# Kernel tuning notes

Hardware: AMD Instinct MI355X
Metric: run time of the kernel (lower is better)

The kernel has to match this reference:

```python
import jax, jax.numpy as jnp
import numpy as np

B, T, H, U, F, K, M = 64, 2048, 1024, 128, 32, 31, 512
PAD = 2 * (K - 1) // 2  # dilation=2, 'same' padding = 30


def setup_inputs() -> dict:
    key = jax.random.key(0)
    ks = jax.random.split(key, 10)
    s = lambda d: 1.0 / np.sqrt(d)
    return {
        "query": jax.random.normal(ks[0], (B, 1, H), dtype=jnp.float32),
        "state": jax.random.uniform(ks[1], (B, T), dtype=jnp.float32),
        "prev_cum": jnp.zeros((B, T), dtype=jnp.float32),
        "memory": jax.random.normal(ks[2], (B, T, M), dtype=jnp.float32),
        "Wq": jax.random.normal(ks[3], (H, U), dtype=jnp.float32) * s(H),
        "bq": jnp.zeros((U,), dtype=jnp.float32),
        "Wm": jax.random.normal(ks[4], (M, U), dtype=jnp.float32) * s(M),
        "bm": jnp.zeros((U,), dtype=jnp.float32),
        "Wl": jax.random.normal(ks[5], (F, U), dtype=jnp.float32) * s(F),
        "bl": jnp.zeros((U,), dtype=jnp.float32),
        "We": jax.random.normal(ks[6], (U, U), dtype=jnp.float32) * s(U),
        "be": jnp.zeros((U,), dtype=jnp.float32),
        "va": jax.random.normal(ks[7], (U,), dtype=jnp.float32),
        "conv_w": jax.random.normal(ks[8], (F, 1, K), dtype=jnp.float32) * s(K),
        "conv_b": jnp.zeros((F,), dtype=jnp.float32),
    }


def reference(query, state, prev_cum, memory, Wq, bq, Wm, bm, Wl, bl, We, be, va, conv_w, conv_b):
    # query projection, keep first time step: [B,1,U]
    pq = (query @ Wq + bq)[:, 0:1, :]
    # processed memory (done in initialize() in torch): [B,T,U]
    pm = memory @ Wm + bm
    # location features: dilated conv over previous alignment, 'same' length
    x = state[:, None, :]  # [B,1,T]
    f = jax.lax.conv_general_dilated(
        x, conv_w, window_strides=(1,), padding=[(PAD, PAD)],
        rhs_dilation=(2,), dimension_numbers=("NCH", "OIH", "NCH"),
    ) + conv_b[None, :, None]                     # [B,F,T]
    pl = jnp.transpose(f, (0, 2, 1)) @ Wl + bl    # [B,T,U]
    # additive energy with extra linear + v_a reduction: [B,T]
    energy = jnp.sum(va * jnp.tanh((pq + pl + pm) @ We + be), axis=2)
    # smoothing (sigmoid) normalization instead of softmax
    sg = jax.nn.sigmoid(energy)
    alignment = sg / jnp.sum(sg, axis=-1, keepdims=True)  # [B,T]
    cum = prev_cum + alignment  # cumulate_weights=True
    # context over PROCESSED memory, matching self.memoery usage: [B,1,U]
    context = cum[:, None, :] @ pm
    return context
```

## Files before the change

### kernel.cpp

```cpp
#include <hip/hip_runtime.h>

#define Bv 64
#define Tv 2048
#define Hv 1024
#define Uv 128
#define Mv 512

typedef __bf16 bf16x8 __attribute__((ext_vector_type(8)));
typedef float f32x4 __attribute__((ext_vector_type(4)));

union U4BF { uint4 u; bf16x8 b; };

#define MFMA(a, b, c) __builtin_amdgcn_mfma_f32_16x16x32_bf16((a), (b), (c), 0, 0, 0)

__device__ __forceinline__ unsigned short f2bf(float f) {
  __bf16 h = (__bf16)f;
  return __builtin_bit_cast(unsigned short, h);
}
__device__ __forceinline__ unsigned int pack2(unsigned short lo, unsigned short hi) {
  return (unsigned int)lo | ((unsigned int)hi << 16);
}

__global__ __launch_bounds__(128) void k1_kernel(const float* __restrict__ query,
                                                 const float* __restrict__ Wq,
                                                 const float* __restrict__ bq,
                                                 const float* __restrict__ Wl,
                                                 const float* __restrict__ bl,
                                                 const float* __restrict__ conv_w,
                                                 const float* __restrict__ conv_b,
                                                 float* __restrict__ pq,
                                                 float* __restrict__ W2,
                                                 float* __restrict__ bias2) {
  const int bx = blockIdx.x;
  const int u = threadIdx.x;
  if (bx < 512) {
    const int b = bx >> 3, c = bx & 7;
    float acc = (c == 0) ? bq[u] : 0.0f;
    const float* q  = query + b * Hv + c * 128;
    const float* wq = Wq + (size_t)c * 128 * Uv;
    #pragma unroll 8
    for (int h = 0; h < 128; ++h) acc = fmaf(q[h], wq[h * Uv + u], acc);
    unsafeAtomicAdd(&pq[b * Uv + u], acc);
  } else {
    float wl[32];
    #pragma unroll
    for (int f = 0; f < 32; ++f) wl[f] = Wl[f * Uv + u];
    for (int k = 0; k < 31; ++k) {
      float acc = 0.0f;
      #pragma unroll
      for (int f = 0; f < 32; ++f) acc = fmaf(conv_w[f * 31 + k], wl[f], acc);
      W2[k * Uv + u] = acc;
    }
    float acc = bl[u];
    #pragma unroll
    for (int f = 0; f < 32; ++f) acc = fmaf(conv_b[f], wl[f], acc);
    bias2[u] = acc;
  }
}

__global__ __launch_bounds__(256) void k2_kernel(const float* __restrict__ pq,
                                                 const float* __restrict__ bias2,
                                                 const float* __restrict__ bm,
                                                 const float* __restrict__ be,
                                                 const float* __restrict__ We,
                                                 const float* __restrict__ W2,
                                                 float* __restrict__ qe,
                                                 float* __restrict__ w3tmp) {
  const int gtid = blockIdx.x * 256 + threadIdx.x;
  const int r = gtid >> 7, n = gtid & 127;
  if (r < 64) {
    float acc = be[n];
    for (int u = 0; u < Uv; ++u)
      acc = fmaf(pq[r * Uv + u] + bias2[u] + bm[u], We[u * Uv + n], acc);
    qe[r * Uv + n] = acc;
  } else {
    const int w = r - 64;
    float acc = 0.0f;
    if (w < 31) {
      for (int u = 0; u < Uv; ++u) acc = fmaf(W2[w * Uv + u], We[u * Uv + n], acc);
    }
    w3tmp[w * Uv + n] = acc;
  }
}

__global__ __launch_bounds__(256) void k3_kernel(const float* __restrict__ Wm,
                                                 const float* __restrict__ We,
                                                 const float* __restrict__ w3tmp,
                                                 unsigned short* __restrict__ WmF,
                                                 unsigned short* __restrict__ WeF,
                                                 unsigned short* __restrict__ W3F) {
  const int gtid = blockIdx.x * 256 + threadIdx.x;
  const int fid = gtid >> 6, lane = gtid & 63;
  const int quad = lane >> 4, l4 = lane & 15;
  float v[8];
  unsigned short* dst;
  if (fid < 128) {
    const int kc = fid >> 3, uj = fid & 7;
    #pragma unroll
    for (int j = 0; j < 8; ++j) v[j] = Wm[(size_t)(kc * 32 + quad * 8 + j) * Uv + uj * 16 + l4];
    dst = WmF + (size_t)fid * 512 + lane * 8;
  } else if (fid < 160) {
    const int f2 = fid - 128;
    const int kc = f2 >> 3, nj = f2 & 7;
    #pragma unroll
    for (int j = 0; j < 8; ++j) v[j] = We[(size_t)(kc * 32 + quad * 8 + j) * Uv + nj * 16 + l4];
    dst = WeF + (size_t)f2 * 512 + lane * 8;
  } else {
    const int nj = fid - 160;
    #pragma unroll
    for (int j = 0; j < 8; ++j) v[j] = w3tmp[(quad * 8 + j) * Uv + nj * 16 + l4];
    dst = W3F + (size_t)nj * 512 + lane * 8;
  }
  uint4 o;
  o.x = pack2(f2bf(v[0]), f2bf(v[1]));
  o.y = pack2(f2bf(v[2]), f2bf(v[3]));
  o.z = pack2(f2bf(v[4]), f2bf(v[5]));
  o.w = pack2(f2bf(v[6]), f2bf(v[7]));
  *(uint4*)dst = o;
}

__global__ __launch_bounds__(256) void main_kernel(
    const float* __restrict__ memory, const unsigned short* __restrict__ WmF,
    const unsigned short* __restrict__ WeF, const unsigned short* __restrict__ W3F,
    const float* __restrict__ qe, const float* __restrict__ state,
    const float* __restrict__ prev_cum, const float* __restrict__ bm,
    const float* __restrict__ va,
    float* __restrict__ P0, float* __restrict__ P1, float* __restrict__ Ssg) {
  const int tid = threadIdx.x;
  const int lane = tid & 63, wid = tid >> 6;
  const int l4 = lane & 15, quad = lane >> 4;
  const int wt = wid >> 1, wu = wid & 1;
  const int b = blockIdx.y, t0 = blockIdx.x * 64;

  __shared__ float sState[124];
  __shared__ float sPc[64];
  __shared__ float sBm[128];
  __shared__ float sVa[128];
  __shared__ float sSg[64];
  __shared__ float blkP0[128], blkP1[128];
  __shared__ float blkSsg;
  __shared__ __align__(16) unsigned short sS[64 * 144];

  for (int i = tid; i < 124; i += 256) {
    int t = t0 - 30 + i;
    sState[i] = (t >= 0 && t < Tv) ? state[b * Tv + t] : 0.0f;
  }
  if (tid < 64) sPc[tid] = prev_cum[b * Tv + t0 + tid];
  for (int i = tid; i < 128; i += 256) {
    sBm[i] = bm[i]; sVa[i] = va[i]; blkP0[i] = 0.0f; blkP1[i] = 0.0f;
  }
  if (tid == 0) blkSsg = 0.0f;

  f32x4 acc[2][4];
  #pragma unroll
  for (int ti = 0; ti < 2; ++ti)
    #pragma unroll
    for (int uj = 0; uj < 4; ++uj) acc[ti][uj] = (f32x4){0.f, 0.f, 0.f, 0.f};

  const float* aBase = memory + ((size_t)b * Tv + t0 + wt * 32 + l4) * Mv + quad * 8;
  const unsigned short* bBase = WmF + (size_t)(wu * 4) * 512 + lane * 8;

  for (int kc = 0; kc < 16; ++kc) {
    float4 a0 = *(const float4*)(aBase + kc * 32);
    float4 a1 = *(const float4*)(aBase + kc * 32 + 4);
    float4 a2 = *(const float4*)(aBase + (size_t)16 * Mv + kc * 32);
    float4 a3 = *(const float4*)(aBase + (size_t)16 * Mv + kc * 32 + 4);
    U4BF bf[4];
    #pragma unroll
    for (int uj = 0; uj < 4; ++uj)
      bf[uj].u = *(const uint4*)(bBase + (size_t)(kc * 8 + uj) * 512);
    bf16x8 af0, af1;
    af0[0] = (__bf16)a0.x; af0[1] = (__bf16)a0.y; af0[2] = (__bf16)a0.z; af0[3] = (__bf16)a0.w;
    af0[4] = (__bf16)a1.x; af0[5] = (__bf16)a1.y; af0[6] = (__bf16)a1.z; af0[7] = (__bf16)a1.w;
    af1[0] = (__bf16)a2.x; af1[1] = (__bf16)a2.y; af1[2] = (__bf16)a2.z; af1[3] = (__bf16)a2.w;
    af1[4] = (__bf16)a3.x; af1[5] = (__bf16)a3.y; af1[6] = (__bf16)a3.z; af1[7] = (__bf16)a3.w;
    #pragma unroll
    for (int uj = 0; uj < 4; ++uj) {
      acc[0][uj] = MFMA(af0, bf[uj].b, acc[0][uj]);
      acc[1][uj] = MFMA(af1, bf[uj].b, acc[1][uj]);
    }
  }

  #pragma unroll
  for (int ti = 0; ti < 2; ++ti) {
    const int rowb = wt * 32 + ti * 16 + quad * 4;
    #pragma unroll
    for (int uj = 0; uj < 4; ++uj) {
      const int col = wu * 64 + uj * 16 + l4;
      #pragma unroll
      for (int r = 0; r < 4; ++r) sS[(rowb + r) * 144 + col] = f2bf(acc[ti][uj][r]);
    }
  }
  __syncthreads();

  const int w = wid;
  f32x4 e[8];
  #pragma unroll
  for (int nj = 0; nj < 8; ++nj) {
    float qv = qe[b * Uv + nj * 16 + l4];
    e[nj] = (f32x4){qv, qv, qv, qv};
  }
  bf16x8 a2f;
  #pragma unroll
  for (int j = 0; j < 8; ++j) {
    int k = quad * 8 + j;
    float v = (k < 31) ? sState[(w * 16 + l4) + 2 * k] : 0.0f;
    a2f[j] = (__bf16)v;
  }
  #pragma unroll
  for (int nj = 0; nj < 8; ++nj) {
    U4BF bb; bb.u = *(const uint4*)(W3F + (size_t)nj * 512 + lane * 8);
    e[nj] = MFMA(a2f, bb.b, e[nj]);
  }
  #pragma unroll
  for (int ks = 0; ks < 4; ++ks) {
    U4BF au;
    au.u = *(const uint4*)&sS[(w * 16 + l4) * 144 + ks * 32 + quad * 8];
    #pragma unroll
    for (int nj = 0; nj < 8; ++nj) {
      U4BF bb; bb.u = *(const uint4*)(WeF + (size_t)(ks * 8 + nj) * 512 + lane * 8);
      e[nj] = MFMA(au.b, bb.b, e[nj]);
    }
  }
  float p[4] = {0.f, 0.f, 0.f, 0.f};
  #pragma unroll
  for (int nj = 0; nj < 8; ++nj) {
    float vav = sVa[nj * 16 + l4];
    #pragma unroll
    for (int r = 0; r < 4; ++r) p[r] = fmaf(vav, tanhf(e[nj][r]), p[r]);
  }
  #pragma unroll
  for (int off = 1; off <= 8; off <<= 1) {
    #pragma unroll
    for (int r = 0; r < 4; ++r) p[r] += __shfl_xor(p[r], off, 64);
  }
  float sgv4[4], sgsum = 0.f;
  #pragma unroll
  for (int r = 0; r < 4; ++r) {
    sgv4[r] = 1.0f / (1.0f + expf(-p[r]));
    sgsum += sgv4[r];
  }
  if (l4 == 0) {
    #pragma unroll
    for (int r = 0; r < 4; ++r) sSg[w * 16 + quad * 4 + r] = sgv4[r];
    atomicAdd(&blkSsg, sgsum);
  }
  __syncthreads();

  float sgl[8], pcl[8];
  #pragma unroll
  for (int ti = 0; ti < 2; ++ti)
    #pragma unroll
    for (int r = 0; r < 4; ++r) {
      int row = wt * 32 + ti * 16 + quad * 4 + r;
      sgl[ti * 4 + r] = sSg[row];
      pcl[ti * 4 + r] = sPc[row];
    }
  #pragma unroll
  for (int uj = 0; uj < 4; ++uj) {
    const int col = wu * 64 + uj * 16 + l4;
    const float bmv = sBm[col];
    float c0 = 0.f, c1 = 0.f;
    #pragma unroll
    for (int ti = 0; ti < 2; ++ti)
      #pragma unroll
      for (int r = 0; r < 4; ++r) {
        float pmv = acc[ti][uj][r] + bmv;
        c0 = fmaf(pcl[ti * 4 + r], pmv, c0);
        c1 = fmaf(sgl[ti * 4 + r], pmv, c1);
      }
    c0 += __shfl_xor(c0, 16, 64); c0 += __shfl_xor(c0, 32, 64);
    c1 += __shfl_xor(c1, 16, 64); c1 += __shfl_xor(c1, 32, 64);
    if (quad == 0) {
      atomicAdd(&blkP0[col], c0);
      atomicAdd(&blkP1[col], c1);
    }
  }
  __syncthreads();
  if (tid < 128) {
    unsafeAtomicAdd(&P0[b * Uv + tid], blkP0[tid]);
    unsafeAtomicAdd(&P1[b * Uv + tid], blkP1[tid]);
  }
  if (tid == 0) unsafeAtomicAdd(&Ssg[b], blkSsg);
}

__global__ __launch_bounds__(128) void finish_kernel(const float* __restrict__ P0,
                                                     const float* __restrict__ P1,
                                                     const float* __restrict__ Ssg,
                                                     float* __restrict__ out) {
  const int b = blockIdx.x, u = threadIdx.x;
  out[b * Uv + u] = P0[b * Uv + u] + P1[b * Uv + u] / Ssg[b];
}

extern "C" void kernel_launch(void* const* d_in, const int* in_sizes, int n_in,
                              void* d_out, int out_size, void* d_ws, size_t ws_size,
                              hipStream_t stream) {
  (void)in_sizes; (void)n_in; (void)out_size; (void)ws_size;
  const float* query    = (const float*)d_in[0];
  const float* state    = (const float*)d_in[1];
  const float* prev_cum = (const float*)d_in[2];
  const float* memory   = (const float*)d_in[3];
  const float* Wq       = (const float*)d_in[4];
  const float* bq       = (const float*)d_in[5];
  const float* Wm       = (const float*)d_in[6];
  const float* bm       = (const float*)d_in[7];
  const float* Wl       = (const float*)d_in[8];
  const float* bl       = (const float*)d_in[9];
  const float* We       = (const float*)d_in[10];
  const float* be       = (const float*)d_in[11];
  const float* va       = (const float*)d_in[12];
  const float* conv_w   = (const float*)d_in[13];
  const float* conv_b   = (const float*)d_in[14];

  float* ws = (float*)d_ws;
  float* P0    = ws;
  float* P1    = ws + 8192;
  float* Ssg   = ws + 16384;
  float* pq    = ws + 16448;
  float* W2    = ws + 24640;
  float* bias2 = ws + 28608;
  float* qe    = ws + 28736;
  float* w3tmp = ws + 36928;
  unsigned short* WmF = (unsigned short*)(ws + 41024);
  unsigned short* WeF = (unsigned short*)(ws + 73792);
  unsigned short* W3F = (unsigned short*)(ws + 81984);

  hipMemsetAsync(d_ws, 0, 24640 * sizeof(float), stream);

  k1_kernel<<<513, 128, 0, stream>>>(query, Wq, bq, Wl, bl, conv_w, conv_b, pq, W2, bias2);
  k2_kernel<<<48, 256, 0, stream>>>(pq, bias2, bm, be, We, W2, qe, w3tmp);
  k3_kernel<<<42, 256, 0, stream>>>(Wm, We, w3tmp, WmF, WeF, W3F);
  main_kernel<<<dim3(Tv / 64, Bv), 256, 0, stream>>>(
      memory, WmF, WeF, W3F, qe, state, prev_cum, bm, va, P0, P1, Ssg);
  finish_kernel<<<Bv, 128, 0, stream>>>(P0, P1, Ssg, (float*)d_out);
}
```

Before: 465.4 us.

## Merge prep kernels, fuse finish via last-block counter, double-buffer GEMM loads

Replaces the memset and three setup kernels with a single prep kernel that also zeroes the accumulation workspace. The separate finish kernel is removed: each batch row counts finished blocks with an atomic counter, and the last block writes the output. The main GEMM loop now double-buffers memory and weight loads in registers. It also prefetches the W3 and qe operands, shrinks the LDS row padding, and uses fast exp-based tanh and sigmoid. The aim is fewer launches and better latency hiding, at the cost of higher register pressure and slightly lower transcendental accuracy.

```diff
diff --git a/kernel.cpp b/kernel.cpp
--- a/kernel.cpp
+++ b/kernel.cpp
@@ -8,9 +8,7 @@
 
 typedef __bf16 bf16x8 __attribute__((ext_vector_type(8)));
 typedef float f32x4 __attribute__((ext_vector_type(4)));
-
 union U4BF { uint4 u; bf16x8 b; };
-
 #define MFMA(a, b, c) __builtin_amdgcn_mfma_f32_16x16x32_bf16((a), (b), (c), 0, 0, 0)
 
 __device__ __forceinline__ unsigned short f2bf(float f) {
@@ -20,112 +18,119 @@
 __device__ __forceinline__ unsigned int pack2(unsigned short lo, unsigned short hi) {
   return (unsigned int)lo | ((unsigned int)hi << 16);
 }
-
-__global__ __launch_bounds__(128) void k1_kernel(const float* __restrict__ query,
-                                                 const float* __restrict__ Wq,
-                                                 const float* __restrict__ bq,
-                                                 const float* __restrict__ Wl,
-                                                 const float* __restrict__ bl,
-                                                 const float* __restrict__ conv_w,
-                                                 const float* __restrict__ conv_b,
-                                                 float* __restrict__ pq,
-                                                 float* __restrict__ W2,
-                                                 float* __restrict__ bias2) {
-  const int bx = blockIdx.x;
-  const int u = threadIdx.x;
-  if (bx < 512) {
-    const int b = bx >> 3, c = bx & 7;
-    float acc = (c == 0) ? bq[u] : 0.0f;
-    const float* q  = query + b * Hv + c * 128;
-    const float* wq = Wq + (size_t)c * 128 * Uv;
-    #pragma unroll 8
-    for (int h = 0; h < 128; ++h) acc = fmaf(q[h], wq[h * Uv + u], acc);
-    unsafeAtomicAdd(&pq[b * Uv + u], acc);
+__device__ __forceinline__ float fast_tanh(float x) {
+  x = fminf(fmaxf(x, -15.0f), 15.0f);
+  float e = __expf(2.0f * x);
+  return (e - 1.0f) / (e + 1.0f);
+}
+
+__global__ __launch_bounds__(256) void prep_kernel(
+    const float* __restrict__ query, const float* __restrict__ Wq,
+    const float* __restrict__ bq, const float* __restrict__ Wl,
+    const float* __restrict__ bl, const float* __restrict__ conv_w,
+    const float* __restrict__ conv_b, const float* __restrict__ bm,
+    const float* __restrict__ be, const float* __restrict__ We,
+    const float* __restrict__ Wm,
+    float* __restrict__ qe, unsigned short* __restrict__ W3F,
+    unsigned short* __restrict__ WmF, unsigned short* __restrict__ WeF,
+    float* __restrict__ zeroRegion) {
+  const int bx = blockIdx.x, tid = threadIdx.x;
+  if (bx < 64) {
+    const int b = bx;
+    __shared__ float part[256];
+    __shared__ float svec[128];
+    const int u = tid & 127, half = tid >> 7;
+    float acc = 0.0f;
+    const float* q  = query + b * Hv + half * 512;
+    const float* wq = Wq + (size_t)(half * 512) * Uv + u;
+    for (int h = 0; h < 512; ++h) acc = fmaf(q[h], wq[(size_t)h * Uv], acc);
+    part[tid] = acc;
+    __syncthreads();
+    if (tid < 128) {
+      float pq = part[tid] + part[tid + 128] + bq[tid];
+      float b2 = bl[tid];
+      #pragma unroll
+      for (int f = 0; f < 32; ++f) b2 = fmaf(conv_b[f], Wl[f * Uv + tid], b2);
+      svec[tid] = pq + b2 + bm[tid];
+    }
+    __syncthreads();
+    const int n = tid & 127;
+    float acc2 = 0.0f;
+    const float* we = We + (size_t)(half * 64) * Uv + n;
+    for (int uu = 0; uu < 64; ++uu) acc2 = fmaf(svec[half * 64 + uu], we[(size_t)uu * Uv], acc2);
+    part[tid] = acc2;
+    __syncthreads();
+    if (tid < 128) qe[b * Uv + tid] = part[tid] + part[tid + 128] + be[tid];
+  } else if (bx == 64) {
+    __shared__ float sW2[31 * 128];
+    __shared__ float sW3[32 * 128];
+    for (int idx = tid; idx < 31 * 128; idx += 256) {
+      int k = idx >> 7, uu = idx & 127;
+      float a = 0.0f;
+      #pragma unroll
+      for (int f = 0; f < 32; ++f) a = fmaf(conv_w[f * 31 + k], Wl[f * Uv + uu], a);
+      sW2[idx] = a;
+    }
+    __syncthreads();
+    for (int idx = tid; idx < 32 * 128; idx += 256) {
+      int k = idx >> 7, n = idx & 127;
+      float a = 0.0f;
+      if (k < 31) {
+        for (int uu = 0; uu < 128; ++uu) a = fmaf(sW2[k * 128 + uu], We[(size_t)uu * Uv + n], a);
+      }
+      sW3[idx] = a;
+    }
+    __syncthreads();
+    for (int s = tid; s < 512; s += 256) {
+      int nj = s >> 6, lane = s & 63, quad = lane >> 4, l4 = lane & 15;
+      float v[8];
+      #pragma unroll
+      for (int j = 0; j < 8; ++j) v[j] = sW3[(quad * 8 + j) * 128 + nj * 16 + l4];
+      uint4 o;
+      o.x = pack2(f2bf(v[0]), f2bf(v[1])); o.y = pack2(f2bf(v[2]), f2bf(v[3]));
+      o.z = pack2(f2bf(v[4]), f2bf(v[5])); o.w = pack2(f2bf(v[6]), f2bf(v[7]));
+      *(uint4*)(W3F + (size_t)nj * 512 + lane * 8) = o;
+    }
+  } else if (bx < 97) {
+    const int fid = (bx - 65) * 4 + (tid >> 6);
+    const int lane = tid & 63, quad = lane >> 4, l4 = lane & 15;
+    const int kc = fid >> 3, uj = fid & 7;
+    float v[8];
+    #pragma unroll
+    for (int j = 0; j < 8; ++j) v[j] = Wm[(size_t)(kc * 32 + quad * 8 + j) * Uv + uj * 16 + l4];
+    uint4 o;
+    o.x = pack2(f2bf(v[0]), f2bf(v[1])); o.y = pack2(f2bf(v[2]), f2bf(v[3]));
+    o.z = pack2(f2bf(v[4]), f2bf(v[5])); o.w = pack2(f2bf(v[6]), f2bf(v[7]));
+    *(uint4*)(WmF + (size_t)fid * 512 + lane * 8) = o;
+  } else if (bx < 105) {
+    const int f2 = (bx - 97) * 4 + (tid >> 6);
+    const int lane = tid & 63, quad = lane >> 4, l4 = lane & 15;
+    const int ks = f2 >> 3, nj = f2 & 7;
+    float v[8];
+    #pragma unroll
+    for (int j = 0; j < 8; ++j) v[j] = We[(size_t)(ks * 32 + quad * 8 + j) * Uv + nj * 16 + l4];
+    uint4 o;
+    o.x = pack2(f2bf(v[0]), f2bf(v[1])); o.y = pack2(f2bf(v[2]), f2bf(v[3]));
+    o.z = pack2(f2bf(v[4]), f2bf(v[5])); o.w = pack2(f2bf(v[6]), f2bf(v[7]));
+    *(uint4*)(WeF + (size_t)f2 * 512 + lane * 8) = o;
   } else {
-    float wl[32];
-    #pragma unroll
-    for (int f = 0; f < 32; ++f) wl[f] = Wl[f * Uv + u];
-    for (int k = 0; k < 31; ++k) {
-      float acc = 0.0f;
-      #pragma unroll
-      for (int f = 0; f < 32; ++f) acc = fmaf(conv_w[f * 31 + k], wl[f], acc);
-      W2[k * Uv + u] = acc;
-    }
-    float acc = bl[u];
-    #pragma unroll
-    for (int f = 0; f < 32; ++f) acc = fmaf(conv_b[f], wl[f], acc);
-    bias2[u] = acc;
-  }
-}
-
-__global__ __launch_bounds__(256) void k2_kernel(const float* __restrict__ pq,
-                                                 const float* __restrict__ bias2,
-                                                 const float* __restrict__ bm,
-                                                 const float* __restrict__ be,
-                                                 const float* __restrict__ We,
-                                                 const float* __restrict__ W2,
-                                                 float* __restrict__ qe,
-                                                 float* __restrict__ w3tmp) {
-  const int gtid = blockIdx.x * 256 + threadIdx.x;
-  const int r = gtid >> 7, n = gtid & 127;
-  if (r < 64) {
-    float acc = be[n];
-    for (int u = 0; u < Uv; ++u)
-      acc = fmaf(pq[r * Uv + u] + bias2[u] + bm[u], We[u * Uv + n], acc);
-    qe[r * Uv + n] = acc;
-  } else {
-    const int w = r - 64;
-    float acc = 0.0f;
-    if (w < 31) {
-      for (int u = 0; u < Uv; ++u) acc = fmaf(W2[w * Uv + u], We[u * Uv + n], acc);
-    }
-    w3tmp[w * Uv + n] = acc;
-  }
-}
-
-__global__ __launch_bounds__(256) void k3_kernel(const float* __restrict__ Wm,
-                                                 const float* __restrict__ We,
-                                                 const float* __restrict__ w3tmp,
-                                                 unsigned short* __restrict__ WmF,
-                                                 unsigned short* __restrict__ WeF,
-                                                 unsigned short* __restrict__ W3F) {
-  const int gtid = blockIdx.x * 256 + threadIdx.x;
-  const int fid = gtid >> 6, lane = gtid & 63;
-  const int quad = lane >> 4, l4 = lane & 15;
-  float v[8];
-  unsigned short* dst;
-  if (fid < 128) {
-    const int kc = fid >> 3, uj = fid & 7;
-    #pragma unroll
-    for (int j = 0; j < 8; ++j) v[j] = Wm[(size_t)(kc * 32 + quad * 8 + j) * Uv + uj * 16 + l4];
-    dst = WmF + (size_t)fid * 512 + lane * 8;
-  } else if (fid < 160) {
-    const int f2 = fid - 128;
-    const int kc = f2 >> 3, nj = f2 & 7;
-    #pragma unroll
-    for (int j = 0; j < 8; ++j) v[j] = We[(size_t)(kc * 32 + quad * 8 + j) * Uv + nj * 16 + l4];
-    dst = WeF + (size_t)f2 * 512 + lane * 8;
-  } else {
-    const int nj = fid - 160;
-    #pragma unroll
-    for (int j = 0; j < 8; ++j) v[j] = w3tmp[(quad * 8 + j) * Uv + nj * 16 + l4];
-    dst = W3F + (size_t)nj * 512 + lane * 8;
-  }
-  uint4 o;
-  o.x = pack2(f2bf(v[0]), f2bf(v[1]));
-  o.y = pack2(f2bf(v[2]), f2bf(v[3]));
-  o.z = pack2(f2bf(v[4]), f2bf(v[5]));
-  o.w = pack2(f2bf(v[6]), f2bf(v[7]));
-  *(uint4*)dst = o;
-}
-
-__global__ __launch_bounds__(256) void main_kernel(
+    const int base = (bx - 105) * 2048 + tid * 8;
+    if (base < 16512) {
+      float4 z = {0.f, 0.f, 0.f, 0.f};
+      *(float4*)(zeroRegion + base) = z;
+      *(float4*)(zeroRegion + base + 4) = z;
+    }
+  }
+}
+
+__global__ __launch_bounds__(256, 4) void main_kernel(
     const float* __restrict__ memory, const unsigned short* __restrict__ WmF,
     const unsigned short* __restrict__ WeF, const unsigned short* __restrict__ W3F,
     const float* __restrict__ qe, const float* __restrict__ state,
     const float* __restrict__ prev_cum, const float* __restrict__ bm,
     const float* __restrict__ va,
-    float* __restrict__ P0, float* __restrict__ P1, float* __restrict__ Ssg) {
+    float* __restrict__ P0, float* __restrict__ P1, float* __restrict__ Ssg,
+    int* __restrict__ cnt, float* __restrict__ out) {
   const int tid = threadIdx.x;
   const int lane = tid & 63, wid = tid >> 6;
   const int l4 = lane & 15, quad = lane >> 4;
@@ -139,16 +144,15 @@
   __shared__ float sSg[64];
   __shared__ float blkP0[128], blkP1[128];
   __shared__ float blkSsg;
-  __shared__ __align__(16) unsigned short sS[64 * 144];
+  __shared__ int sDone;
+  __shared__ __align__(16) unsigned short sS[64 * 136];
 
   for (int i = tid; i < 124; i += 256) {
     int t = t0 - 30 + i;
     sState[i] = (t >= 0 && t < Tv) ? state[b * Tv + t] : 0.0f;
   }
   if (tid < 64) sPc[tid] = prev_cum[b * Tv + t0 + tid];
-  for (int i = tid; i < 128; i += 256) {
-    sBm[i] = bm[i]; sVa[i] = va[i]; blkP0[i] = 0.0f; blkP1[i] = 0.0f;
-  }
+  if (tid < 128) { sBm[tid] = bm[tid]; sVa[tid] = va[tid]; blkP0[tid] = 0.0f; blkP1[tid] = 0.0f; }
   if (tid == 0) blkSsg = 0.0f;
 
   f32x4 acc[2][4];
@@ -157,28 +161,54 @@
     #pragma unroll
     for (int uj = 0; uj < 4; ++uj) acc[ti][uj] = (f32x4){0.f, 0.f, 0.f, 0.f};
 
-  const float* aBase = memory + ((size_t)b * Tv + t0 + wt * 32 + l4) * Mv + quad * 8;
-  const unsigned short* bBase = WmF + (size_t)(wu * 4) * 512 + lane * 8;
-
+  const float* aPtr = memory + ((size_t)b * Tv + t0 + wt * 32 + l4) * Mv + quad * 8;
+  const unsigned short* bPtr = WmF + (size_t)(wu * 4) * 512 + lane * 8;
+
+  float4 Abuf[2][4];
+  uint4  Bbuf[2][4];
+  Abuf[0][0] = *(const float4*)(aPtr);
+  Abuf[0][1] = *(const float4*)(aPtr + 4);
+  Abuf[0][2] = *(const float4*)(aPtr + (size_t)16 * Mv);
+  Abuf[0][3] = *(const float4*)(aPtr + (size_t)16 * Mv + 4);
+  #pragma unroll
+  for (int j = 0; j < 4; ++j) Bbuf[0][j] = *(const uint4*)(bPtr + (size_t)j * 512);
+
+  #pragma unroll
   for (int kc = 0; kc < 16; ++kc) {
-    float4 a0 = *(const float4*)(aBase + kc * 32);
-    float4 a1 = *(const float4*)(aBase + kc * 32 + 4);
-    float4 a2 = *(const float4*)(aBase + (size_t)16 * Mv + kc * 32);
-    float4 a3 = *(const float4*)(aBase + (size_t)16 * Mv + kc * 32 + 4);
-    U4BF bf[4];
-    #pragma unroll
-    for (int uj = 0; uj < 4; ++uj)
-      bf[uj].u = *(const uint4*)(bBase + (size_t)(kc * 8 + uj) * 512);
+    const int cur = kc & 1, nxt = cur ^ 1;
+    if (kc < 15) {
+      const float* ap = aPtr + (kc + 1) * 32;
+      Abuf[nxt][0] = *(const float4*)(ap);
+      Abuf[nxt][1] = *(const float4*)(ap + 4);
+      Abuf[nxt][2] = *(const float4*)(ap + (size_t)16 * Mv);
+      Abuf[nxt][3] = *(const float4*)(ap + (size_t)16 * Mv + 4);
+      #pragma unroll
+      for (int j = 0; j < 4; ++j)
+        Bbuf[nxt][j] = *(const uint4*)(bPtr + (size_t)((kc + 1) * 8 + j) * 512);
+    }
     bf16x8 af0, af1;
-    af0[0] = (__bf16)a0.x; af0[1] = (__bf16)a0.y; af0[2] = (__bf16)a0.z; af0[3] = (__bf16)a0.w;
-    af0[4] = (__bf16)a1.x; af0[5] = (__bf16)a1.y; af0[6] = (__bf16)a1.z; af0[7] = (__bf16)a1.w;
-    af1[0] = (__bf16)a2.x; af1[1] = (__bf16)a2.y; af1[2] = (__bf16)a2.z; af1[3] = (__bf16)a2.w;
-    af1[4] = (__bf16)a3.x; af1[5] = (__bf16)a3.y; af1[6] = (__bf16)a3.z; af1[7] = (__bf16)a3.w;
+    af0[0] = (__bf16)Abuf[cur][0].x; af0[1] = (__bf16)Abuf[cur][0].y;
+    af0[2] = (__bf16)Abuf[cur][0].z; af0[3] = (__bf16)Abuf[cur][0].w;
+    af0[4] = (__bf16)Abuf[cur][1].x; af0[5] = (__bf16)Abuf[cur][1].y;
+    af0[6] = (__bf16)Abuf[cur][1].z; af0[7] = (__bf16)Abuf[cur][1].w;
+    af1[0] = (__bf16)Abuf[cur][2].x; af1[1] = (__bf16)Abuf[cur][2].y;
+    af1[2] = (__bf16)Abuf[cur][2].z; af1[3] = (__bf16)Abuf[cur][2].w;
+    af1[4] = (__bf16)Abuf[cur][3].x; af1[5] = (__bf16)Abuf[cur][3].y;
+    af1[6] = (__bf16)Abuf[cur][3].z; af1[7] = (__bf16)Abuf[cur][3].w;
     #pragma unroll
     for (int uj = 0; uj < 4; ++uj) {
-      acc[0][uj] = MFMA(af0, bf[uj].b, acc[0][uj]);
-      acc[1][uj] = MFMA(af1, bf[uj].b, acc[1][uj]);
-    }
+      U4BF bb; bb.u = Bbuf[cur][uj];
+      acc[0][uj] = MFMA(af0, bb.b, acc[0][uj]);
+      acc[1][uj] = MFMA(af1, bb.b, acc[1][uj]);
+    }
+  }
+
+  float qv[8];
+  U4BF w3[8];
+  #pragma unroll
+  for (int nj = 0; nj < 8; ++nj) {
+    qv[nj] = qe[b * Uv + nj * 16 + l4];
+    w3[nj].u = *(const uint4*)(W3F + (size_t)nj * 512 + lane * 8);
   }
 
   #pragma unroll
@@ -188,34 +218,27 @@
     for (int uj = 0; uj < 4; ++uj) {
       const int col = wu * 64 + uj * 16 + l4;
       #pragma unroll
-      for (int r = 0; r < 4; ++r) sS[(rowb + r) * 144 + col] = f2bf(acc[ti][uj][r]);
-    }
-  }
-  __syncthreads();
-
-  const int w = wid;
+      for (int r = 0; r < 4; ++r) sS[(rowb + r) * 136 + col] = f2bf(acc[ti][uj][r]);
+    }
+  }
+  __syncthreads();
+
   f32x4 e[8];
   #pragma unroll
-  for (int nj = 0; nj < 8; ++nj) {
-    float qv = qe[b * Uv + nj * 16 + l4];
-    e[nj] = (f32x4){qv, qv, qv, qv};
-  }
+  for (int nj = 0; nj < 8; ++nj) e[nj] = (f32x4){qv[nj], qv[nj], qv[nj], qv[nj]};
   bf16x8 a2f;
   #pragma unroll
   for (int j = 0; j < 8; ++j) {
     int k = quad * 8 + j;
-    float v = (k < 31) ? sState[(w * 16 + l4) + 2 * k] : 0.0f;
+    float v = (k < 31) ? sState[(wid * 16 + l4) + 2 * k] : 0.0f;
     a2f[j] = (__bf16)v;
   }
   #pragma unroll
-  for (int nj = 0; nj < 8; ++nj) {
-    U4BF bb; bb.u = *(const uint4*)(W3F + (size_t)nj * 512 + lane * 8);
-    e[nj] = MFMA(a2f, bb.b, e[nj]);
-  }
+  for (int nj = 0; nj < 8; ++nj) e[nj] = MFMA(a2f, w3[nj].b, e[nj]);
   #pragma unroll
   for (int ks = 0; ks < 4; ++ks) {
     U4BF au;
-    au.u = *(const uint4*)&sS[(w * 16 + l4) * 144 + ks * 32 + quad * 8];
+    au.u = *(const uint4*)&sS[(wid * 16 + l4) * 136 + ks * 32 + quad * 8];
     #pragma unroll
     for (int nj = 0; nj < 8; ++nj) {
       U4BF bb; bb.u = *(const uint4*)(WeF + (size_t)(ks * 8 + nj) * 512 + lane * 8);
@@ -227,22 +250,23 @@
   for (int nj = 0; nj < 8; ++nj) {
     float vav = sVa[nj * 16 + l4];
     #pragma unroll
-    for (int r = 0; r < 4; ++r) p[r] = fmaf(vav, tanhf(e[nj][r]), p[r]);
+    for (int r = 0; r < 4; ++r) p[r] = fmaf(vav, fast_tanh(e[nj][r]), p[r]);
   }
   #pragma unroll
   for (int off = 1; off <= 8; off <<= 1) {
     #pragma unroll
     for (int r = 0; r < 4; ++r) p[r] += __shfl_xor(p[r], off, 64);
   }
-  float sgv4[4], sgsum = 0.f;
+  float sgsum = 0.f;
+  float sgv4[4];
   #pragma unroll
   for (int r = 0; r < 4; ++r) {
-    sgv4[r] = 1.0f / (1.0f + expf(-p[r]));
+    sgv4[r] = 1.0f / (1.0f + __expf(-p[r]));
     sgsum += sgv4[r];
   }
   if (l4 == 0) {
     #pragma unroll
-    for (int r = 0; r < 4; ++r) sSg[w * 16 + quad * 4 + r] = sgv4[r];
+    for (int r = 0; r < 4; ++r) sSg[wid * 16 + quad * 4 + r] = sgv4[r];
     atomicAdd(&blkSsg, sgsum);
   }
   __syncthreads();
@@ -282,14 +306,22 @@
     unsafeAtomicAdd(&P1[b * Uv + tid], blkP1[tid]);
   }
   if (tid == 0) unsafeAtomicAdd(&Ssg[b], blkSsg);
-}
-
-__global__ __launch_bounds__(128) void finish_kernel(const float* __restrict__ P0,
-                                                     const float* __restrict__ P1,
-                                                     const float* __restrict__ Ssg,
-                                                     float* __restrict__ out) {
-  const int b = blockIdx.x, u = threadIdx.x;
-  out[b * Uv + u] = P0[b * Uv + u] + P1[b * Uv + u] / Ssg[b];
+  __syncthreads();
+
+  if (tid == 0) {
+    __threadfence();
+    sDone = __hip_atomic_fetch_add(&cnt[b], 1, __ATOMIC_ACQ_REL, __HIP_MEMORY_SCOPE_AGENT);
+  }
+  __syncthreads();
+  if (sDone == 31) {
+    __threadfence();
+    if (tid < 128) {
+      float p0 = __hip_atomic_load(&P0[b * Uv + tid], __ATOMIC_ACQUIRE, __HIP_MEMORY_SCOPE_AGENT);
+      float p1 = __hip_atomic_load(&P1[b * Uv + tid], __ATOMIC_ACQUIRE, __HIP_MEMORY_SCOPE_AGENT);
+      float ss = __hip_atomic_load(&Ssg[b], __ATOMIC_ACQUIRE, __HIP_MEMORY_SCOPE_AGENT);
+      out[b * Uv + tid] = p0 + p1 / ss;
+    }
+  }
 }
 
 extern "C" void kernel_launch(void* const* d_in, const int* in_sizes, int n_in,
@@ -313,24 +345,18 @@
   const float* conv_b   = (const float*)d_in[14];
 
   float* ws = (float*)d_ws;
-  float* P0    = ws;
-  float* P1    = ws + 8192;
-  float* Ssg   = ws + 16384;
-  float* pq    = ws + 16448;
-  float* W2    = ws + 24640;
-  float* bias2 = ws + 28608;
-  float* qe    = ws + 28736;
-  float* w3tmp = ws + 36928;
-  unsigned short* WmF = (unsigned short*)(ws + 41024);
-  unsigned short* WeF = (unsigned short*)(ws + 73792);
-  unsigned short* W3F = (unsigned short*)(ws + 81984);
-
-  hipMemsetAsync(d_ws, 0, 24640 * sizeof(float), stream);
-
-  k1_kernel<<<513, 128, 0, stream>>>(query, Wq, bq, Wl, bl, conv_w, conv_b, pq, W2, bias2);
-  k2_kernel<<<48, 256, 0, stream>>>(pq, bias2, bm, be, We, W2, qe, w3tmp);
-  k3_kernel<<<42, 256, 0, stream>>>(Wm, We, w3tmp, WmF, WeF, W3F);
+  float* P0  = ws;
+  float* P1  = ws + 8192;
+  float* Ssg = ws + 16384;
+  int*   cnt = (int*)(ws + 16448);
+  float* qe  = ws + 16512;
+  unsigned short* W3F = (unsigned short*)(ws + 24704);
+  unsigned short* WmF = (unsigned short*)(ws + 26752);
+  unsigned short* WeF = (unsigned short*)(ws + 59520);
+
+  prep_kernel<<<114, 256, 0, stream>>>(query, Wq, bq, Wl, bl, conv_w, conv_b,
+                                       bm, be, We, Wm, qe, W3F, WmF, WeF, ws);
   main_kernel<<<dim3(Tv / 64, Bv), 256, 0, stream>>>(
-      memory, WmF, WeF, W3F, qe, state, prev_cum, bm, va, P0, P1, Ssg);
-  finish_kernel<<<Bv, 128, 0, stream>>>(P0, P1, Ssg, (float*)d_out);
-}
+      memory, WmF, WeF, W3F, qe, state, prev_cum, bm, va, P0, P1, Ssg, cnt,
+      (float*)d_out);
+}
```

Measured after the change: 672.6 us. 1.45x slower.
